# Kernel tuning notes

Hardware: AMD Instinct MI355X
Metric: run time of the kernel (lower is better)

Reference implementation:

```python
import jax, jax.numpy as jnp
import numpy as np

N, B, D, K_IN, P = 64, 256, 1792, 35, 10
EPS = 1e-5


def setup_inputs() -> dict:
    key = jax.random.key(0)
    ks = jax.random.split(key, 8)
    s_tok = 1.0 / np.sqrt(K_IN)
    s_net = 1.0 / np.sqrt(D)
    return {
        "X": jax.random.normal(ks[0], (N, B, D), dtype=jnp.float32),
        "task_id": jax.random.normal(ks[1], (B, K_IN), dtype=jnp.float32),
        # tokens: Linear(35, 10*1792)
        "W_tok": jax.random.uniform(ks[2], (P * D, K_IN), jnp.float32, -s_tok, s_tok),
        "b_tok": jax.random.uniform(ks[3], (P * D,), jnp.float32, -s_tok, s_tok),
        # ptokens: Linear(35, 1792)
        "W_ptok": jax.random.uniform(ks[4], (D, K_IN), jnp.float32, -s_tok, s_tok),
        "b_ptok": jax.random.uniform(ks[5], (D,), jnp.float32, -s_tok, s_tok),
        # LayerNorm(1792)
        "gamma": jnp.ones((D,), jnp.float32),
        "beta": jnp.zeros((D,), jnp.float32),
        # net: Linear(1792, 10)
        "W_net": jax.random.uniform(ks[6], (P, D), jnp.float32, -s_net, s_net),
        "b_net": jax.random.uniform(ks[7], (P,), jnp.float32, -s_net, s_net),
    }


def _layernorm(x, gamma, beta):
    mu = jnp.mean(x, axis=-1, keepdims=True)
    var = jnp.mean(jnp.square(x - mu), axis=-1, keepdims=True)
    return (x - mu) * jax.lax.rsqrt(var + EPS) * gamma + beta


def reference(X, task_id, W_tok, b_tok, W_ptok, b_ptok, gamma, beta, W_net, b_net):
    # ptokens(task_id): (b, D); identical across n, so compute once and broadcast.
    ptok = task_id @ W_ptok.T + b_ptok                       # (b, D)
    task_token = _layernorm(ptok[None, :, :] + X, gamma, beta)  # (n, b, D)
    # net -> sigmoid: per-token mixing weights over P prompts.
    weight = jax.nn.sigmoid(task_token @ W_net.T + b_net)    # (n, b, P)
    # tokens(task_id): (b, P, D); identical across n, broadcast in einsum.
    prompt_bank = (task_id @ W_tok.T + b_tok).reshape(B, P, D)  # (b, P, D)
    prompt = jnp.einsum("nbp,bpd->nbd", weight, prompt_bank)  # (n, b, D)
    return X + prompt
```

## Files before the change

### kernel.cpp

```cpp
#include <hip/hip_runtime.h>
#include <hip/hip_bf16.h>

#define NN 64
#define BB 256
#define DD 1792
#define KK 35
#define PP 10
#define DQ 448
#define GR 8
#define NGRP 28

__device__ __forceinline__ float group16_sum_dpp(float x) {
    asm("v_add_f32_dpp %0, %0, %0 row_shr:1 row_mask:0xf bank_mask:0xf bound_ctrl:0" : "+v"(x));
    asm("v_add_f32_dpp %0, %0, %0 row_shr:2 row_mask:0xf bank_mask:0xf bound_ctrl:0" : "+v"(x));
    asm("v_add_f32_dpp %0, %0, %0 row_shr:4 row_mask:0xf bank_mask:0xf bound_ctrl:0" : "+v"(x));
    asm("v_add_f32_dpp %0, %0, %0 row_shr:8 row_mask:0xf bank_mask:0xf bound_ctrl:0" : "+v"(x));
    return x;
}

__global__ void prep_gf(const float* __restrict__ gamma, const float* __restrict__ beta,
                        const float* __restrict__ Wnet, const float* __restrict__ bnet,
                        float* __restrict__ GF, float* __restrict__ SG, float* __restrict__ ZC) {
    const int p = blockIdx.x;
    const int tid = threadIdx.x;
    float sg = 0.f, sb = 0.f;
#pragma unroll
    for (int j = 0; j < 7; ++j) {
        int d = j * 256 + tid;
        float wv = Wnet[p * DD + d];
        float g = gamma[d] * wv;
        GF[p * DD + d] = g;
        sg += g;
        sb += beta[d] * wv;
    }
#pragma unroll
    for (int off = 32; off > 0; off >>= 1) {
        sg += __shfl_xor(sg, off);
        sb += __shfl_xor(sb, off);
    }
    __shared__ float rs[4][2];
    if ((tid & 63) == 0) { rs[tid >> 6][0] = sg; rs[tid >> 6][1] = sb; }
    __syncthreads();
    if (tid == 0) {
        float a = 0.f, c = 0.f;
#pragma unroll
        for (int w = 0; w < 4; ++w) { a += rs[w][0]; c += rs[w][1]; }
        SG[p] = a;
        ZC[p] = c + bnet[p];
    }
}

__global__ void prep_bank(const float* __restrict__ task,
                          const float* __restrict__ Wtok, const float* __restrict__ btok,
                          const float* __restrict__ Wptok, const float* __restrict__ bptok,
                          float* __restrict__ bank, float* __restrict__ ptok) {
    __shared__ float ti[32 * KK];
    const int tid = threadIdx.x;
    const int b0 = blockIdx.y * 32;
    for (int i = tid; i < 32 * KK; i += 256) ti[i] = task[b0 * KK + i];

    const int r = blockIdx.x * 256 + tid;
    const bool isbank = (r < PP * DD);
    const int rr = isbank ? r : (r - PP * DD);
    const float* __restrict__ W = isbank ? Wtok : Wptok;
    const float bias = isbank ? btok[r] : bptok[rr];

    float w[KK];
#pragma unroll
    for (int k = 0; k < KK; ++k) w[k] = W[rr * KK + k];

    __syncthreads();
#pragma unroll 1
    for (int bb = 0; bb < 32; ++bb) {
        float acc = bias;
#pragma unroll
        for (int k = 0; k < KK; ++k) acc = fmaf(ti[bb * KK + k], w[k], acc);
        const int b = b0 + bb;
        if (isbank) bank[b * (PP * DD) + r] = acc;
        else        ptok[b * DD + rr]       = acc;
    }
}

__global__ __launch_bounds__(448) void fused_persist(
    const float* __restrict__ X, const float* __restrict__ BANK,
    const float* __restrict__ PTOK, const float* __restrict__ GF,
    const float* __restrict__ SG, const float* __restrict__ ZC,
    float* __restrict__ OUT) {
    const int tid  = threadIdx.x;
    const int b    = blockIdx.x >> 1;
    const int g0   = (blockIdx.x & 1) * 4;

    const float4* __restrict__ X4 = (const float4*)X;
    const float4* __restrict__ B4 = (const float4*)BANK;
    const float4* __restrict__ G4 = (const float4*)GF;
    const float4* __restrict__ P4 = (const float4*)PTOK;
    float4* __restrict__ O4 = (float4*)OUT;

    __shared__ float red[GR][NGRP][12];
    __shared__ float wlds[GR][PP];

    const float4 ptk = P4[(size_t)b * DQ + tid];
    float4 gf[PP];
#pragma unroll
    for (int p = 0; p < PP; ++p) gf[p] = G4[(size_t)p * DQ + tid];
    float4 bk[PP];
#pragma unroll
    for (int p = 0; p < PP; ++p) bk[p] = B4[((size_t)b * PP + p) * DQ + tid];

    const bool writer = ((tid & 15) == 15);
    const int g16 = tid >> 4;

    float4 x0[GR], x1[GR];

#define BURST(XN, GN)                                                              \
    {                                                                              \
        _Pragma("unroll")                                                          \
        for (int r = 0; r < GR; ++r)                                               \
            XN[r] = X4[((size_t)((GN) * GR + r) * BB + b) * DQ + tid];             \
        __builtin_amdgcn_sched_barrier(0);                                         \
    }

#define BARRIER_RAW()                                                              \
    asm volatile("s_waitcnt lgkmcnt(0)" ::: "memory");                             \
    __builtin_amdgcn_sched_barrier(0);                                             \
    __builtin_amdgcn_s_barrier();                                                  \
    __builtin_amdgcn_sched_barrier(0);

#define PHASE1(XC)                                                                 \
    {                                                                              \
        _Pragma("unroll")                                                          \
        for (int r = 0; r < GR; ++r) {                                             \
            float4 t;                                                              \
            t.x = XC[r].x + ptk.x; t.y = XC[r].y + ptk.y;                          \
            t.z = XC[r].z + ptk.z; t.w = XC[r].w + ptk.w;                          \
            float s1 = t.x + t.y + t.z + t.w;                                      \
            float s2 = t.x * t.x;                                                  \
            s2 = fmaf(t.y, t.y, s2); s2 = fmaf(t.z, t.z, s2);                      \
            s2 = fmaf(t.w, t.w, s2);                                               \
            float a[PP];                                                           \
            _Pragma("unroll")                                                      \
            for (int p = 0; p < PP; ++p) {                                         \
                float v = t.x * gf[p].x;                                           \
                v = fmaf(t.y, gf[p].y, v);                                         \
                v = fmaf(t.z, gf[p].z, v);                                         \
                v = fmaf(t.w, gf[p].w, v);                                         \
                a[p] = v;                                                          \
            }                                                                      \
            s1 = group16_sum_dpp(s1);                                              \
            s2 = group16_sum_dpp(s2);                                              \
            _Pragma("unroll")                                                      \
            for (int p = 0; p < PP; ++p) a[p] = group16_sum_dpp(a[p]);             \
            if (writer) {                                                          \
                float4* dst = (float4*)&red[r][g16][0];                            \
                dst[0] = make_float4(s1, s2, a[0], a[1]);                          \
                dst[1] = make_float4(a[2], a[3], a[4], a[5]);                      \
                dst[2] = make_float4(a[6], a[7], a[8], a[9]);                      \
            }                                                                      \
        }                                                                          \
    }

#define FINALIZE()                                                                 \
    if (tid < GR * 16) {                                                           \
        const int row = tid >> 4;                                                  \
        const int v = tid & 15;                                                    \
        float f = 0.f;                                                             \
        if (v < 12) {                                                              \
            _Pragma("unroll")                                                      \
            for (int q = 0; q < NGRP; ++q) f += red[row][q][v];                    \
        }                                                                          \
        const int bse = (tid & 63) & ~15;                                          \
        const float mu = __shfl(f, bse)     * (1.0f / (float)DD);                  \
        const float ms = __shfl(f, bse + 1) * (1.0f / (float)DD);                  \
        const float istd = rsqrtf(ms - mu * mu + 1e-5f);                           \
        if (v >= 2 && v < 12) {                                                    \
            const int p = v - 2;                                                   \
            const float z = istd * (f - mu * SG[p]) + ZC[p];                       \
            wlds[row][p] = 1.0f / (1.0f + __expf(-z));                             \
        }                                                                          \
    }

#define PHASE2(XC, GN)                                                             \
    {                                                                              \
        _Pragma("unroll")                                                          \
        for (int r = 0; r < GR; ++r) {                                             \
            float4 acc = XC[r];                                                    \
            _Pragma("unroll")                                                      \
            for (int p = 0; p < PP; ++p) {                                         \
                const float wv = wlds[r][p];                                       \
                acc.x = fmaf(wv, bk[p].x, acc.x);                                  \
                acc.y = fmaf(wv, bk[p].y, acc.y);                                  \
                acc.z = fmaf(wv, bk[p].z, acc.z);                                  \
                acc.w = fmaf(wv, bk[p].w, acc.w);                                  \
            }                                                                      \
            O4[((size_t)((GN) * GR + r) * BB + b) * DQ + tid] = acc;               \
        }                                                                          \
    }

#define GROUP(XC, XN, GN, DO_NEXT)                                                 \
    if (DO_NEXT) { BURST(XN, (GN) + 1) }                                           \
    PHASE1(XC)                                                                     \
    BARRIER_RAW()                                                                  \
    FINALIZE()                                                                     \
    BARRIER_RAW()                                                                  \
    PHASE2(XC, GN)

    BURST(x0, g0 + 0)

    GROUP(x0, x1, g0 + 0, true)
    GROUP(x1, x0, g0 + 1, true)
    GROUP(x0, x1, g0 + 2, true)
    GROUP(x1, x0, g0 + 3, false)

#undef GROUP
#undef PHASE2
#undef FINALIZE
#undef PHASE1
#undef BARRIER_RAW
#undef BURST
}

extern "C" void kernel_launch(void* const* d_in, const int* in_sizes, int n_in,
                              void* d_out, int out_size, void* d_ws, size_t ws_size,
                              hipStream_t stream) {
    const float* X     = (const float*)d_in[0];
    const float* task  = (const float*)d_in[1];
    const float* Wtok  = (const float*)d_in[2];
    const float* btok  = (const float*)d_in[3];
    const float* Wptok = (const float*)d_in[4];
    const float* bptok = (const float*)d_in[5];
    const float* gamma = (const float*)d_in[6];
    const float* beta  = (const float*)d_in[7];
    const float* Wnet  = (const float*)d_in[8];
    const float* bnet  = (const float*)d_in[9];
    float* out = (float*)d_out;

    float* ws = (float*)d_ws;
    float* bank = ws;
    float* ptok = bank + (size_t)BB * PP * DD;
    float* GF   = ptok + (size_t)BB * DD;
    float* SG   = GF + PP * DD;
    float* ZC   = SG + PP;

    prep_gf<<<PP, 256, 0, stream>>>(gamma, beta, Wnet, bnet, GF, SG, ZC);
    prep_bank<<<dim3(77, 8), 256, 0, stream>>>(task, Wtok, btok, Wptok, bptok, bank, ptok);
    fused_persist<<<2 * BB, 448, 0, stream>>>(X, bank, ptok, GF, SG, ZC, out);
}
```

Measured before the change: 86.49 us.

## Software-pipeline LayerNorm groups with triple-buffered X and double-buffered reductions

Each block now handles all 8 row-groups for one batch index instead of splitting them across two blocks, so the grid is halved. The schedule uses triple-buffered X registers and double-buffered LDS reduction and weight buffers, so one barrier per group is removed and phase 2 of group g overlaps phase 1 of group g+1. The cost is higher register pressure (launch_bounds 448,1) and only 256 blocks, which reduces occupancy and the parallelism available to hide memory latency.

```diff
diff --git a/kernel.cpp b/kernel.cpp
--- a/kernel.cpp
+++ b/kernel.cpp
@@ -81,14 +81,13 @@
     }
 }
 
-__global__ __launch_bounds__(448) void fused_persist(
+__global__ __launch_bounds__(448, 1) void fused_pipe(
     const float* __restrict__ X, const float* __restrict__ BANK,
     const float* __restrict__ PTOK, const float* __restrict__ GF,
     const float* __restrict__ SG, const float* __restrict__ ZC,
     float* __restrict__ OUT) {
-    const int tid  = threadIdx.x;
-    const int b    = blockIdx.x >> 1;
-    const int g0   = (blockIdx.x & 1) * 4;
+    const int tid = threadIdx.x;
+    const int b = blockIdx.x;
 
     const float4* __restrict__ X4 = (const float4*)X;
     const float4* __restrict__ B4 = (const float4*)BANK;
@@ -96,8 +95,8 @@
     const float4* __restrict__ P4 = (const float4*)PTOK;
     float4* __restrict__ O4 = (float4*)OUT;
 
-    __shared__ float red[GR][NGRP][12];
-    __shared__ float wlds[GR][PP];
+    __shared__ float red[2][GR][NGRP][12];
+    __shared__ float wlds[2][GR][PP];
 
     const float4 ptk = P4[(size_t)b * DQ + tid];
     float4 gf[PP];
@@ -110,7 +109,7 @@
     const bool writer = ((tid & 15) == 15);
     const int g16 = tid >> 4;
 
-    float4 x0[GR], x1[GR];
+    float4 x0[GR], x1[GR], x2[GR];
 
 #define BURST(XN, GN)                                                              \
     {                                                                              \
@@ -126,7 +125,7 @@
     __builtin_amdgcn_s_barrier();                                                  \
     __builtin_amdgcn_sched_barrier(0);
 
-#define PHASE1(XC)                                                                 \
+#define PHASE1(XC, RB)                                                             \
     {                                                                              \
         _Pragma("unroll")                                                          \
         for (int r = 0; r < GR; ++r) {                                             \
@@ -151,7 +150,7 @@
             _Pragma("unroll")                                                      \
             for (int p = 0; p < PP; ++p) a[p] = group16_sum_dpp(a[p]);             \
             if (writer) {                                                          \
-                float4* dst = (float4*)&red[r][g16][0];                            \
+                float4* dst = (float4*)&red[RB][r][g16][0];                        \
                 dst[0] = make_float4(s1, s2, a[0], a[1]);                          \
                 dst[1] = make_float4(a[2], a[3], a[4], a[5]);                      \
                 dst[2] = make_float4(a[6], a[7], a[8], a[9]);                      \
@@ -159,14 +158,14 @@
         }                                                                          \
     }
 
-#define FINALIZE()                                                                 \
+#define FINALIZE(RB)                                                               \
     if (tid < GR * 16) {                                                           \
         const int row = tid >> 4;                                                  \
         const int v = tid & 15;                                                    \
         float f = 0.f;                                                             \
         if (v < 12) {                                                              \
             _Pragma("unroll")                                                      \
-            for (int q = 0; q < NGRP; ++q) f += red[row][q][v];                    \
+            for (int q = 0; q < NGRP; ++q) f += red[RB][row][q][v];                \
         }                                                                          \
         const int bse = (tid & 63) & ~15;                                          \
         const float mu = __shfl(f, bse)     * (1.0f / (float)DD);                  \
@@ -175,18 +174,18 @@
         if (v >= 2 && v < 12) {                                                    \
             const int p = v - 2;                                                   \
             const float z = istd * (f - mu * SG[p]) + ZC[p];                       \
-            wlds[row][p] = 1.0f / (1.0f + __expf(-z));                             \
-        }                                                                          \
-    }
-
-#define PHASE2(XC, GN)                                                             \
+            wlds[RB][row][p] = 1.0f / (1.0f + __expf(-z));                         \
+        }                                                                          \
+    }
+
+#define PHASE2(XC, WB, GN)                                                         \
     {                                                                              \
         _Pragma("unroll")                                                          \
         for (int r = 0; r < GR; ++r) {                                             \
             float4 acc = XC[r];                                                    \
             _Pragma("unroll")                                                      \
             for (int p = 0; p < PP; ++p) {                                         \
-                const float wv = wlds[r][p];                                       \
+                const float wv = wlds[WB][r][p];                                   \
                 acc.x = fmaf(wv, bk[p].x, acc.x);                                  \
                 acc.y = fmaf(wv, bk[p].y, acc.y);                                  \
                 acc.z = fmaf(wv, bk[p].z, acc.z);                                  \
@@ -196,22 +195,18 @@
         }                                                                          \
     }
 
-#define GROUP(XC, XN, GN, DO_NEXT)                                                 \
-    if (DO_NEXT) { BURST(XN, (GN) + 1) }                                           \
-    PHASE1(XC)                                                                     \
-    BARRIER_RAW()                                                                  \
-    FINALIZE()                                                                     \
-    BARRIER_RAW()                                                                  \
-    PHASE2(XC, GN)
-
-    BURST(x0, g0 + 0)
-
-    GROUP(x0, x1, g0 + 0, true)
-    GROUP(x1, x0, g0 + 1, true)
-    GROUP(x0, x1, g0 + 2, true)
-    GROUP(x1, x0, g0 + 3, false)
-
-#undef GROUP
+    BURST(x0, 0)
+
+    BURST(x1, 1) PHASE1(x0, 0) BARRIER_RAW() FINALIZE(0)
+    BURST(x2, 2) PHASE1(x1, 1) BARRIER_RAW() FINALIZE(1) PHASE2(x0, 0, 0)
+    BURST(x0, 3) PHASE1(x2, 0) BARRIER_RAW() FINALIZE(0) PHASE2(x1, 1, 1)
+    BURST(x1, 4) PHASE1(x0, 1) BARRIER_RAW() FINALIZE(1) PHASE2(x2, 0, 2)
+    BURST(x2, 5) PHASE1(x1, 0) BARRIER_RAW() FINALIZE(0) PHASE2(x0, 1, 3)
+    BURST(x0, 6) PHASE1(x2, 1) BARRIER_RAW() FINALIZE(1) PHASE2(x1, 0, 4)
+    BURST(x1, 7) PHASE1(x0, 0) BARRIER_RAW() FINALIZE(0) PHASE2(x2, 1, 5)
+    PHASE1(x1, 1) BARRIER_RAW() FINALIZE(1) PHASE2(x0, 0, 6)
+    BARRIER_RAW() PHASE2(x1, 1, 7)
+
 #undef PHASE2
 #undef FINALIZE
 #undef PHASE1
@@ -243,5 +238,5 @@
 
     prep_gf<<<PP, 256, 0, stream>>>(gamma, beta, Wnet, bnet, GF, SG, ZC);
     prep_bank<<<dim3(77, 8), 256, 0, stream>>>(task, Wtok, btok, Wptok, bptok, bank, ptok);
-    fused_persist<<<2 * BB, 448, 0, stream>>>(X, bank, ptok, GF, SG, ZC, out);
-}
+    fused_pipe<<<BB, 448, 0, stream>>>(X, bank, ptok, GF, SG, ZC, out);
+}
```

Measured after the change: 77.19 us. 1.12x faster.
